# Optimization experiments

Measured on AMD Instinct MI355X. Metric: run time of the kernel, lower is better.

## Reference

```python
import jax, jax.numpy as jnp
import numpy as np

MARGIN = 2.0   # self.m
SCALE = 30.0   # cosine-head logit scale


def setup_inputs() -> dict:
    key = jax.random.key(0)
    k1, k2, k3 = jax.random.split(key, 3)
    B, D, C = 8192, 256, 5994
    emb = jax.random.normal(k1, (B, D), dtype=jnp.float32)
    W = jax.random.normal(k2, (C, D), dtype=jnp.float32) * 0.05
    y = jax.random.randint(k3, (B,), 0, C, dtype=jnp.int32)
    # first half domain 0 (main), second half domain 1 (target)
    y_d = jnp.concatenate([jnp.zeros(B // 2, jnp.int32), jnp.ones(B // 2, jnp.int32)])
    return {"emb": emb, "W": W, "y": y, "y_d": y_d}


def _clf_head(emb, W, y):
    # cosine-similarity classifier + cross-entropy (standard ASV clf head)
    e = emb / (jnp.linalg.norm(emb, axis=1, keepdims=True) + 1e-12)
    w = W / (jnp.linalg.norm(W, axis=1, keepdims=True) + 1e-12)
    logits = SCALE * (e @ w.T)                     # [B, C]
    logp = jax.nn.log_softmax(logits, axis=-1)
    loss = -jnp.mean(jnp.take_along_axis(logp, y[:, None], axis=1))
    acc = jnp.mean((jnp.argmax(logits, axis=-1) == y).astype(jnp.float32))
    return loss, acc


def reference(emb, W, y, y_d):
    B, D = emb.shape
    H = B // 2
    idx = jnp.arange(B)
    # faithful scatter: domain-0 rows -> main_emb[i]; domain-1 rows -> target_emb[i % H]
    # out-of-range sentinel H is dropped (rows with wrong domain stay zero)
    main_idx = jnp.where(y_d == 0, idx, H)
    tgt_idx = jnp.where(y_d != 0, idx % H, H)
    main_emb = jnp.zeros((H, D), emb.dtype).at[main_idx].set(emb, mode="drop")
    target_emb = jnp.zeros((H, D), emb.dtype).at[tgt_idx].set(emb, mode="drop")

    loss_c, acc = _clf_head(emb, W, y)

    # pairwise diffs: even rows main[i]-main[(i+1)%H] (label 1), odd rows main[i]-target[i] (label 0)
    pos_diff = main_emb - jnp.roll(main_emb, -1, axis=0)  # [H, D]
    neg_diff = main_emb - target_emb                      # [H, D]
    das_diff = jnp.stack([pos_diff, neg_diff], axis=1).reshape(B, D)
    das_label = jnp.tile(jnp.array([1.0, 0.0], emb.dtype), H)  # [B]

    das_dist = jnp.linalg.norm(das_diff, axis=1)
    das_loss = jnp.mean((1.0 - das_label) * das_dist ** 2
                        + das_label * jnp.maximum(MARGIN - das_dist, 0.0) ** 2)
    das_dist_mean = jnp.mean(jax.lax.stop_gradient(das_dist))
    return (loss_c, das_loss, acc, das_dist_mean)
```

## Files before the change

### kernel.cpp

```cpp
#include <hip/hip_runtime.h>
#include <hip/hip_bf16.h>

#define B_ROWS 8192
#define DIM 256
#define C_CLS 5994
#define N_CHUNK 188
#define NSPL 16
#define NPACK 444
#define NDAS 128
#define NMERGE 512
#define H_HALF 4096
#define SCALE_F 30.0f
#define MAXL 30.0f
#define EXPC 43.2808512266689f

#if defined(__has_builtin)
#if __has_builtin(__builtin_amdgcn_exp2f)
#define EXP2(x) __builtin_amdgcn_exp2f(x)
#endif
#endif
#ifndef EXP2
#define EXP2(x) exp2f(x)
#endif

typedef float f32x16 __attribute__((ext_vector_type(16)));
typedef long long ll;
typedef ll ll2 __attribute__((ext_vector_type(2)));

__global__ __launch_bounds__(256)
void k_pack(const float* __restrict__ emb, const float* __restrict__ W,
            char* __restrict__ en_blk, char* __restrict__ wn_blk,
            float* __restrict__ rne, float* __restrict__ rnw,
            unsigned* __restrict__ cnt) {
  __shared__ float ssm[256];
  __shared__ float rnl[32];
  const int b = blockIdx.x;
  const int t = threadIdx.x;
  if (b == 0 && t == 0) *cnt = 0u;
  const bool isW = b >= (B_ROWS/32);
  const int tile = isW ? b - (B_ROWS/32) : b;
  const int l31 = t & 31;
  const int row = tile*32 + l31;
  const float* __restrict__ src = isW ? W : emb;
  const bool rv = (!isW) || (row < C_CLS);

  float v[4][8];
  float ss = 0.f;
  #pragma unroll
  for (int i=0;i<4;i++) {
    const int d0 = ((t>>6) + i*4)*16 + ((t>>5)&1)*8;
    if (rv) {
      float4 x0 = *(const float4*)(src + (size_t)row*DIM + d0);
      float4 x1 = *(const float4*)(src + (size_t)row*DIM + d0 + 4);
      v[i][0]=x0.x; v[i][1]=x0.y; v[i][2]=x0.z; v[i][3]=x0.w;
      v[i][4]=x1.x; v[i][5]=x1.y; v[i][6]=x1.z; v[i][7]=x1.w;
      ss += x0.x*x0.x + x0.y*x0.y + x0.z*x0.z + x0.w*x0.w
          + x1.x*x1.x + x1.y*x1.y + x1.z*x1.z + x1.w*x1.w;
    } else {
      #pragma unroll
      for (int j=0;j<8;j++) v[i][j] = 0.f;
    }
  }
  ssm[t] = ss;
  __syncthreads();
  if (t < 32) {
    float s = 0.f;
    #pragma unroll
    for (int j=0;j<8;j++) s += ssm[t + j*32];
    float rn = 1.0f/(sqrtf(s) + 1e-12f);
    rnl[t] = rn;
    int rw = tile*32 + t;
    if (!isW) rne[rw] = rn;
    else if (rw < C_CLS) rnw[rw] = rn;
  }
  __syncthreads();
  const float rn = rnl[l31];
  char* __restrict__ dst = (isW ? wn_blk : en_blk) + (size_t)tile*8192;
  #pragma unroll
  for (int i=0;i<4;i++) {
    const int kk = (t>>6) + i*4;
    const int off = (kk>>1)*1024 + ((t>>5)&1)*512 + l31*16 + (kk&1)*8;
    int d0 = 0, d1 = 0;
    d0 = __builtin_amdgcn_cvt_pk_fp8_f32(v[i][0]*rn, v[i][1]*rn, d0, false);
    d0 = __builtin_amdgcn_cvt_pk_fp8_f32(v[i][2]*rn, v[i][3]*rn, d0, true);
    d1 = __builtin_amdgcn_cvt_pk_fp8_f32(v[i][4]*rn, v[i][5]*rn, d1, false);
    d1 = __builtin_amdgcn_cvt_pk_fp8_f32(v[i][6]*rn, v[i][7]*rn, d1, true);
    uint2 u; u.x = (unsigned)d0; u.y = (unsigned)d1;
    *(uint2*)(dst + off) = u;
  }
}

__global__ __launch_bounds__(256)
void k_das(const float* __restrict__ emb, const int* __restrict__ y_d,
           float* __restrict__ dasL, float* __restrict__ dasD) {
  __shared__ float s0[4], s1[4];
  const int wid = threadIdx.x >> 6, lane = threadIdx.x & 63;
  float a2 = 0.f, a3 = 0.f;
  for (int i = blockIdx.x*4 + wid; i < H_HALF; i += NDAS*4) {
    const int j = (i+1) & (H_HALF-1);
    const int di = y_d[i], dj = y_d[j], dih = y_d[i + H_HALF];
    float4 z = {0.f,0.f,0.f,0.f};
    float4 mi = (di==0)  ? *(const float4*)(emb + (size_t)i*DIM + lane*4) : z;
    float4 mj = (dj==0)  ? *(const float4*)(emb + (size_t)j*DIM + lane*4) : z;
    float4 ti = (dih!=0) ? *(const float4*)(emb + (size_t)(i+H_HALF)*DIM + lane*4)
                         : ((di!=0) ? *(const float4*)(emb + (size_t)i*DIM + lane*4) : z);
    float px = mi.x-mj.x, py = mi.y-mj.y, pz = mi.z-mj.z, pw = mi.w-mj.w;
    float nx = mi.x-ti.x, ny = mi.y-ti.y, nz = mi.z-ti.z, nw = mi.w-ti.w;
    float sp = px*px+py*py+pz*pz+pw*pw;
    float sn = nx*nx+ny*ny+nz*nz+nw*nw;
    #pragma unroll
    for (int off=1; off<64; off<<=1) { sp += __shfl_xor(sp, off); sn += __shfl_xor(sn, off); }
    if (lane == 0) {
      float dp = sqrtf(sp), dn = sqrtf(sn);
      float m = fmaxf(2.0f - dp, 0.f);
      a2 += m*m + dn*dn;
      a3 += dp + dn;
    }
  }
  if (lane == 0) { s0[wid] = a2; s1[wid] = a3; }
  __syncthreads();
  if (threadIdx.x == 0) {
    dasL[blockIdx.x] = s0[0]+s0[1]+s0[2]+s0[3];
    dasD[blockIdx.x] = s1[0]+s1[1]+s1[2]+s1[3];
  }
}

__global__ __launch_bounds__(256, 2)
void k_logits(const char* __restrict__ en_blk, const char* __restrict__ wn_blk,
              float* __restrict__ psum, unsigned* __restrict__ pkey) {
  const int split = blockIdx.x & (NSPL-1);
  const int panel = blockIdx.x / NSPL;
  const int wid  = threadIdx.x >> 6;
  const int lane = threadIdx.x & 63;
  const int l31  = lane & 31;
  const int tile = panel*4 + wid;

  ll2 a[8];
  const char* ab = en_blk + (size_t)tile*8192 + lane*16;
  #pragma unroll
  for (int j=0;j<8;j++) a[j] = *(const ll2*)(ab + j*1024);

  float ssum[16]; unsigned key[16];
  #pragma unroll
  for (int r=0;r<16;r++){ ssum[r]=0.f; key[r]=0u; }

  const int nit = (N_CHUNK - split + NSPL - 1) / NSPL;
  const char* p = wn_blk + (size_t)split*8192 + lane*16;
  const ptrdiff_t STEP = (ptrdiff_t)NSPL*8192;

  ll2 b0[4], b1[4];
  #pragma unroll
  for (int j=0;j<4;j++) b0[j] = *(const ll2*)(p + j*1024);
  #pragma unroll
  for (int j=0;j<4;j++) b1[j] = *(const ll2*)(p + (j+4)*1024);

  unsigned colu = (unsigned)(split*32 + l31);
  for (int it = 0; it < nit-1; ++it) {
    const char* pn = p + STEP;
    f32x16 acc = {};
    #pragma unroll
    for (int j=0;j<4;j++) {
      acc = __builtin_amdgcn_mfma_f32_32x32x16_fp8_fp8(a[j][0], b0[j][0], acc, 0,0,0);
      acc = __builtin_amdgcn_mfma_f32_32x32x16_fp8_fp8(a[j][1], b0[j][1], acc, 0,0,0);
    }
    #pragma unroll
    for (int j=0;j<4;j++) b0[j] = *(const ll2*)(pn + j*1024);
    #pragma unroll
    for (int j=0;j<4;j++) {
      acc = __builtin_amdgcn_mfma_f32_32x32x16_fp8_fp8(a[j+4][0], b1[j][0], acc, 0,0,0);
      acc = __builtin_amdgcn_mfma_f32_32x32x16_fp8_fp8(a[j+4][1], b1[j][1], acc, 0,0,0);
    }
    #pragma unroll
    for (int j=0;j<4;j++) b1[j] = *(const ll2*)(pn + (j+4)*1024);
    #pragma unroll
    for (int r=0;r<16;r++) {
      float x = acc[r];
      ssum[r] += EXP2(fmaf(x, EXPC, -EXPC));
      unsigned ky = (__float_as_uint(x + 2.0f) & 0xFFFFE000u) | colu;
      key[r] = ky > key[r] ? ky : key[r];
    }
    colu += NSPL*32;
    p = pn;
  }
  {
    f32x16 acc = {};
    #pragma unroll
    for (int j=0;j<4;j++) {
      acc = __builtin_amdgcn_mfma_f32_32x32x16_fp8_fp8(a[j][0], b0[j][0], acc, 0,0,0);
      acc = __builtin_amdgcn_mfma_f32_32x32x16_fp8_fp8(a[j][1], b0[j][1], acc, 0,0,0);
    }
    #pragma unroll
    for (int j=0;j<4;j++) {
      acc = __builtin_amdgcn_mfma_f32_32x32x16_fp8_fp8(a[j+4][0], b1[j][0], acc, 0,0,0);
      acc = __builtin_amdgcn_mfma_f32_32x32x16_fp8_fp8(a[j+4][1], b1[j][1], acc, 0,0,0);
    }
    #pragma unroll
    for (int r=0;r<16;r++) {
      float x = acc[r];
      ssum[r] += EXP2(fmaf(x, EXPC, -EXPC));
      unsigned ky = (__float_as_uint(x + 2.0f) & 0xFFFFE000u) | colu;
      key[r] = ky > key[r] ? ky : key[r];
    }
  }

  #pragma unroll
  for (int off=1; off<32; off<<=1) {
    #pragma unroll
    for (int r=0;r<16;r++) {
      ssum[r] += __shfl_xor(ssum[r], off);
      unsigned o = __shfl_xor(key[r], off);
      key[r] = o > key[r] ? o : key[r];
    }
  }
  if (l31 == 0) {
    const int rowbase = tile*32;
    #pragma unroll
    for (int r=0;r<16;r++) {
      int row = rowbase + (r&3) + 8*(r>>2) + 4*(lane>>5);
      psum[(size_t)row*NSPL + split] = ssum[r];
      pkey[(size_t)row*NSPL + split] = key[r];
    }
  }
}

__global__ __launch_bounds__(256)
void k_tail(const float* __restrict__ emb, const float* __restrict__ W,
            const int* __restrict__ y,
            const float* __restrict__ rne, const float* __restrict__ rnw,
            const float* __restrict__ psum, const unsigned* __restrict__ pkey,
            float* __restrict__ lossP, float* __restrict__ corrP,
            const float* __restrict__ dasL, const float* __restrict__ dasD,
            unsigned* __restrict__ cnt, float* __restrict__ out) {
  __shared__ float s0[4], s1[4];
  __shared__ int isLast;
  const int wid = threadIdx.x >> 6, lane = threadIdx.x & 63;
  float lacc = 0.f, cacc = 0.f;
  for (int row = blockIdx.x*4 + wid; row < B_ROWS; row += NMERGE*4) {
    const int yc = y[row];
    float4 e = *(const float4*)(emb + (size_t)row*DIM + lane*4);
    float4 w = *(const float4*)(W + (size_t)yc*DIM + lane*4);
    float d = e.x*w.x + e.y*w.y + e.z*w.z + e.w*w.w;
    #pragma unroll
    for (int off=1; off<64; off<<=1) d += __shfl_xor(d, off);
    float S = 0.f; unsigned km = 0u;
    if (lane < NSPL) {
      S = psum[(size_t)row*NSPL + lane];
      km = pkey[(size_t)row*NSPL + lane];
    }
    #pragma unroll
    for (int off=1; off<NSPL; off<<=1) {
      S += __shfl_xor(S, off);
      unsigned o = __shfl_xor(km, off);
      if (o > km) km = o;
    }
    if (lane == 0) {
      float ly = SCALE_F * d * rne[row] * rnw[yc];
      lacc += MAXL + logf(S) - ly;
      cacc += ((km & 0x1FFFu) == (unsigned)yc) ? 1.f : 0.f;
    }
  }
  if (lane == 0) { s0[wid] = lacc; s1[wid] = cacc; }
  __syncthreads();
  if (threadIdx.x == 0) {
    lossP[blockIdx.x] = s0[0]+s0[1]+s0[2]+s0[3];
    corrP[blockIdx.x] = s1[0]+s1[1]+s1[2]+s1[3];
    __threadfence();
    unsigned done = atomicAdd(cnt, 1u);
    isLast = (done == NMERGE-1u) ? 1 : 0;
  }
  __syncthreads();
  if (isLast) {
    const int t = threadIdx.x;
    float lv = atomicAdd(&lossP[t], 0.f) + atomicAdd(&lossP[t+256], 0.f);
    float cv = atomicAdd(&corrP[t], 0.f) + atomicAdd(&corrP[t+256], 0.f);
    float dl = (t < NDAS) ? atomicAdd((float*)&dasL[t], 0.f) : 0.f;
    float dd = (t < NDAS) ? atomicAdd((float*)&dasD[t], 0.f) : 0.f;
    #pragma unroll
    for (int off=1; off<64; off<<=1) {
      lv += __shfl_xor(lv, off); cv += __shfl_xor(cv, off);
      dl += __shfl_xor(dl, off); dd += __shfl_xor(dd, off);
    }
    __shared__ float r4[4][4];
    if (lane == 0) { r4[wid][0]=lv; r4[wid][1]=cv; r4[wid][2]=dl; r4[wid][3]=dd; }
    __syncthreads();
    if (t == 0) {
      out[0] = (r4[0][0]+r4[1][0]+r4[2][0]+r4[3][0]) * (1.0f/B_ROWS);
      out[1] = (r4[0][2]+r4[1][2]+r4[2][2]+r4[3][2]) * (1.0f/B_ROWS);
      out[2] = (r4[0][1]+r4[1][1]+r4[2][1]+r4[3][1]) * (1.0f/B_ROWS);
      out[3] = (r4[0][3]+r4[1][3]+r4[2][3]+r4[3][3]) * (1.0f/B_ROWS);
    }
  }
}

extern "C" void kernel_launch(void* const* d_in, const int* in_sizes, int n_in,
                              void* d_out, int out_size, void* d_ws, size_t ws_size,
                              hipStream_t stream) {
  const float* emb = (const float*)d_in[0];
  const float* W   = (const float*)d_in[1];
  const int*   y   = (const int*)d_in[2];
  const int*   y_d = (const int*)d_in[3];

  char* ws = (char*)d_ws;
  const size_t EN_OFF   = 0;
  const size_t WN_OFF   = EN_OFF  + (size_t)256*8192;
  const size_t RNE_OFF  = WN_OFF  + (size_t)N_CHUNK*8192;
  const size_t RNW_OFF  = RNE_OFF + (size_t)B_ROWS*4;
  const size_t PSUM_OFF = RNW_OFF + 24064;
  const size_t PKEY_OFF = PSUM_OFF + (size_t)NSPL*B_ROWS*4;
  const size_t LP_OFF   = PKEY_OFF + (size_t)NSPL*B_ROWS*4;
  const size_t CP_OFF   = LP_OFF   + NMERGE*4;
  const size_t DL_OFF   = CP_OFF   + NMERGE*4;
  const size_t DD_OFF   = DL_OFF   + NDAS*4;
  const size_t CNT_OFF  = DD_OFF   + NDAS*4;

  char*     en_blk = ws + EN_OFF;
  char*     wn_blk = ws + WN_OFF;
  float*    rne   = (float*)(ws + RNE_OFF);
  float*    rnw   = (float*)(ws + RNW_OFF);
  float*    psum  = (float*)(ws + PSUM_OFF);
  unsigned* pkey  = (unsigned*)(ws + PKEY_OFF);
  float*    lossP = (float*)(ws + LP_OFF);
  float*    corrP = (float*)(ws + CP_OFF);
  float*    dasL  = (float*)(ws + DL_OFF);
  float*    dasD  = (float*)(ws + DD_OFF);
  unsigned* cnt   = (unsigned*)(ws + CNT_OFF);

  k_pack<<<NPACK, 256, 0, stream>>>(emb, W, en_blk, wn_blk, rne, rnw, cnt);
  k_das<<<NDAS, 256, 0, stream>>>(emb, y_d, dasL, dasD);
  k_logits<<<64*NSPL, 256, 0, stream>>>(en_blk, wn_blk, psum, pkey);
  k_tail<<<NMERGE, 256, 0, stream>>>(emb, W, y, rne, rnw, psum, pkey,
                                     lossP, corrP, dasL, dasD, cnt, (float*)d_out);
}
```

Before: 71.14 us.

## Fuse DAS into pack kernel and capture target logit inside GEMM epilogue

The separate DAS kernel becomes extra blocks appended to the pack kernel, saving one launch and letting both run concurrently. The target-class logit is now taken from the fp8 MFMA accumulator during the logits pass and stored per split, instead of being recomputed in the tail from fp32 emb and W rows plus saved norms. This cuts the tail's global reads and the rne/rnw writes, but adds a compare/select per accumulator element in the hot loop and a third per-split output array. The target logit now carries fp8 precision rather than the previous fp32 dot product.

```diff
diff --git a/kernel.cpp b/kernel.cpp
--- a/kernel.cpp
+++ b/kernel.cpp
@@ -29,14 +29,51 @@
 
 __global__ __launch_bounds__(256)
 void k_pack(const float* __restrict__ emb, const float* __restrict__ W,
+            const int* __restrict__ y_d,
             char* __restrict__ en_blk, char* __restrict__ wn_blk,
-            float* __restrict__ rne, float* __restrict__ rnw,
+            float* __restrict__ dasL, float* __restrict__ dasD,
             unsigned* __restrict__ cnt) {
   __shared__ float ssm[256];
   __shared__ float rnl[32];
+  __shared__ float s0[4], s1[4];
   const int b = blockIdx.x;
   const int t = threadIdx.x;
   if (b == 0 && t == 0) *cnt = 0u;
+
+  if (b >= NPACK) {
+    const int bd = b - NPACK;
+    const int wid = t >> 6, lane = t & 63;
+    float a2 = 0.f, a3 = 0.f;
+    for (int i = bd*4 + wid; i < H_HALF; i += NDAS*4) {
+      const int j = (i+1) & (H_HALF-1);
+      const int di = y_d[i], dj = y_d[j], dih = y_d[i + H_HALF];
+      float4 z = {0.f,0.f,0.f,0.f};
+      float4 mi = (di==0)  ? *(const float4*)(emb + (size_t)i*DIM + lane*4) : z;
+      float4 mj = (dj==0)  ? *(const float4*)(emb + (size_t)j*DIM + lane*4) : z;
+      float4 ti = (dih!=0) ? *(const float4*)(emb + (size_t)(i+H_HALF)*DIM + lane*4)
+                           : ((di!=0) ? *(const float4*)(emb + (size_t)i*DIM + lane*4) : z);
+      float px = mi.x-mj.x, py = mi.y-mj.y, pz = mi.z-mj.z, pw = mi.w-mj.w;
+      float nx = mi.x-ti.x, ny = mi.y-ti.y, nz = mi.z-ti.z, nw = mi.w-ti.w;
+      float sp = px*px+py*py+pz*pz+pw*pw;
+      float sn = nx*nx+ny*ny+nz*nz+nw*nw;
+      #pragma unroll
+      for (int off=1; off<64; off<<=1) { sp += __shfl_xor(sp, off); sn += __shfl_xor(sn, off); }
+      if (lane == 0) {
+        float dp = sqrtf(sp), dn = sqrtf(sn);
+        float m = fmaxf(2.0f - dp, 0.f);
+        a2 += m*m + dn*dn;
+        a3 += dp + dn;
+      }
+    }
+    if (lane == 0) { s0[wid] = a2; s1[wid] = a3; }
+    __syncthreads();
+    if (t == 0) {
+      dasL[bd] = s0[0]+s0[1]+s0[2]+s0[3];
+      dasD[bd] = s1[0]+s1[1]+s1[2]+s1[3];
+    }
+    return;
+  }
+
   const bool isW = b >= (B_ROWS/32);
   const int tile = isW ? b - (B_ROWS/32) : b;
   const int l31 = t & 31;
@@ -67,11 +104,7 @@
     float s = 0.f;
     #pragma unroll
     for (int j=0;j<8;j++) s += ssm[t + j*32];
-    float rn = 1.0f/(sqrtf(s) + 1e-12f);
-    rnl[t] = rn;
-    int rw = tile*32 + t;
-    if (!isW) rne[rw] = rn;
-    else if (rw < C_CLS) rnw[rw] = rn;
+    rnl[t] = 1.0f/(sqrtf(s) + 1e-12f);
   }
   __syncthreads();
   const float rn = rnl[l31];
@@ -90,59 +123,33 @@
   }
 }
 
-__global__ __launch_bounds__(256)
-void k_das(const float* __restrict__ emb, const int* __restrict__ y_d,
-           float* __restrict__ dasL, float* __restrict__ dasD) {
-  __shared__ float s0[4], s1[4];
-  const int wid = threadIdx.x >> 6, lane = threadIdx.x & 63;
-  float a2 = 0.f, a3 = 0.f;
-  for (int i = blockIdx.x*4 + wid; i < H_HALF; i += NDAS*4) {
-    const int j = (i+1) & (H_HALF-1);
-    const int di = y_d[i], dj = y_d[j], dih = y_d[i + H_HALF];
-    float4 z = {0.f,0.f,0.f,0.f};
-    float4 mi = (di==0)  ? *(const float4*)(emb + (size_t)i*DIM + lane*4) : z;
-    float4 mj = (dj==0)  ? *(const float4*)(emb + (size_t)j*DIM + lane*4) : z;
-    float4 ti = (dih!=0) ? *(const float4*)(emb + (size_t)(i+H_HALF)*DIM + lane*4)
-                         : ((di!=0) ? *(const float4*)(emb + (size_t)i*DIM + lane*4) : z);
-    float px = mi.x-mj.x, py = mi.y-mj.y, pz = mi.z-mj.z, pw = mi.w-mj.w;
-    float nx = mi.x-ti.x, ny = mi.y-ti.y, nz = mi.z-ti.z, nw = mi.w-ti.w;
-    float sp = px*px+py*py+pz*pz+pw*pw;
-    float sn = nx*nx+ny*ny+nz*nz+nw*nw;
-    #pragma unroll
-    for (int off=1; off<64; off<<=1) { sp += __shfl_xor(sp, off); sn += __shfl_xor(sn, off); }
-    if (lane == 0) {
-      float dp = sqrtf(sp), dn = sqrtf(sn);
-      float m = fmaxf(2.0f - dp, 0.f);
-      a2 += m*m + dn*dn;
-      a3 += dp + dn;
-    }
-  }
-  if (lane == 0) { s0[wid] = a2; s1[wid] = a3; }
-  __syncthreads();
-  if (threadIdx.x == 0) {
-    dasL[blockIdx.x] = s0[0]+s0[1]+s0[2]+s0[3];
-    dasD[blockIdx.x] = s1[0]+s1[1]+s1[2]+s1[3];
-  }
-}
-
 __global__ __launch_bounds__(256, 2)
 void k_logits(const char* __restrict__ en_blk, const char* __restrict__ wn_blk,
-              float* __restrict__ psum, unsigned* __restrict__ pkey) {
+              const int* __restrict__ y,
+              float* __restrict__ psum, unsigned* __restrict__ pkey,
+              float* __restrict__ lyP) {
   const int split = blockIdx.x & (NSPL-1);
   const int panel = blockIdx.x / NSPL;
   const int wid  = threadIdx.x >> 6;
   const int lane = threadIdx.x & 63;
   const int l31  = lane & 31;
+  const int lh   = lane >> 5;
   const int tile = panel*4 + wid;
+  const int rowbase = tile*32;
 
   ll2 a[8];
   const char* ab = en_blk + (size_t)tile*8192 + lane*16;
   #pragma unroll
   for (int j=0;j<8;j++) a[j] = *(const ll2*)(ab + j*1024);
 
-  float ssum[16]; unsigned key[16];
-  #pragma unroll
-  for (int r=0;r<16;r++){ ssum[r]=0.f; key[r]=0u; }
+  unsigned tcol[16];
+  #pragma unroll
+  for (int r=0;r<16;r++)
+    tcol[r] = (unsigned)y[rowbase + (r&3) + 8*(r>>2) + 4*lh];
+
+  float ssum[16], lyv[16]; unsigned key[16];
+  #pragma unroll
+  for (int r=0;r<16;r++){ ssum[r]=0.f; key[r]=0u; lyv[r]=-3.0e38f; }
 
   const int nit = (N_CHUNK - split + NSPL - 1) / NSPL;
   const char* p = wn_blk + (size_t)split*8192 + lane*16;
@@ -178,6 +185,7 @@
       ssum[r] += EXP2(fmaf(x, EXPC, -EXPC));
       unsigned ky = (__float_as_uint(x + 2.0f) & 0xFFFFE000u) | colu;
       key[r] = ky > key[r] ? ky : key[r];
+      lyv[r] = (colu == tcol[r]) ? x : lyv[r];
     }
     colu += NSPL*32;
     p = pn;
@@ -200,6 +208,7 @@
       ssum[r] += EXP2(fmaf(x, EXPC, -EXPC));
       unsigned ky = (__float_as_uint(x + 2.0f) & 0xFFFFE000u) | colu;
       key[r] = ky > key[r] ? ky : key[r];
+      lyv[r] = (colu == tcol[r]) ? x : lyv[r];
     }
   }
 
@@ -210,24 +219,24 @@
       ssum[r] += __shfl_xor(ssum[r], off);
       unsigned o = __shfl_xor(key[r], off);
       key[r] = o > key[r] ? o : key[r];
+      lyv[r] = fmaxf(lyv[r], __shfl_xor(lyv[r], off));
     }
   }
   if (l31 == 0) {
-    const int rowbase = tile*32;
     #pragma unroll
     for (int r=0;r<16;r++) {
-      int row = rowbase + (r&3) + 8*(r>>2) + 4*(lane>>5);
+      int row = rowbase + (r&3) + 8*(r>>2) + 4*lh;
       psum[(size_t)row*NSPL + split] = ssum[r];
       pkey[(size_t)row*NSPL + split] = key[r];
+      lyP [(size_t)row*NSPL + split] = lyv[r];
     }
   }
 }
 
 __global__ __launch_bounds__(256)
-void k_tail(const float* __restrict__ emb, const float* __restrict__ W,
-            const int* __restrict__ y,
-            const float* __restrict__ rne, const float* __restrict__ rnw,
+void k_tail(const int* __restrict__ y,
             const float* __restrict__ psum, const unsigned* __restrict__ pkey,
+            const float* __restrict__ lyP,
             float* __restrict__ lossP, float* __restrict__ corrP,
             const float* __restrict__ dasL, const float* __restrict__ dasD,
             unsigned* __restrict__ cnt, float* __restrict__ out) {
@@ -236,27 +245,22 @@
   const int wid = threadIdx.x >> 6, lane = threadIdx.x & 63;
   float lacc = 0.f, cacc = 0.f;
   for (int row = blockIdx.x*4 + wid; row < B_ROWS; row += NMERGE*4) {
-    const int yc = y[row];
-    float4 e = *(const float4*)(emb + (size_t)row*DIM + lane*4);
-    float4 w = *(const float4*)(W + (size_t)yc*DIM + lane*4);
-    float d = e.x*w.x + e.y*w.y + e.z*w.z + e.w*w.w;
-    #pragma unroll
-    for (int off=1; off<64; off<<=1) d += __shfl_xor(d, off);
-    float S = 0.f; unsigned km = 0u;
+    float S = 0.f, lym = -3.0e38f; unsigned km = 0u;
     if (lane < NSPL) {
-      S = psum[(size_t)row*NSPL + lane];
-      km = pkey[(size_t)row*NSPL + lane];
+      S   = psum[(size_t)row*NSPL + lane];
+      km  = pkey[(size_t)row*NSPL + lane];
+      lym = lyP [(size_t)row*NSPL + lane];
     }
     #pragma unroll
     for (int off=1; off<NSPL; off<<=1) {
       S += __shfl_xor(S, off);
       unsigned o = __shfl_xor(km, off);
       if (o > km) km = o;
+      lym = fmaxf(lym, __shfl_xor(lym, off));
     }
     if (lane == 0) {
-      float ly = SCALE_F * d * rne[row] * rnw[yc];
-      lacc += MAXL + logf(S) - ly;
-      cacc += ((km & 0x1FFFu) == (unsigned)yc) ? 1.f : 0.f;
+      lacc += MAXL + logf(S) - SCALE_F * lym;
+      cacc += ((km & 0x1FFFu) == (unsigned)y[row]) ? 1.f : 0.f;
     }
   }
   if (lane == 0) { s0[wid] = lacc; s1[wid] = cacc; }
@@ -271,8 +275,8 @@
   __syncthreads();
   if (isLast) {
     const int t = threadIdx.x;
-    float lv = atomicAdd(&lossP[t], 0.f) + atomicAdd(&lossP[t+256], 0.f);
-    float cv = atomicAdd(&corrP[t], 0.f) + atomicAdd(&corrP[t+256], 0.f);
+    float lv = atomicAdd((float*)&lossP[t], 0.f) + atomicAdd((float*)&lossP[t+256], 0.f);
+    float cv = atomicAdd((float*)&corrP[t], 0.f) + atomicAdd((float*)&corrP[t+256], 0.f);
     float dl = (t < NDAS) ? atomicAdd((float*)&dasL[t], 0.f) : 0.f;
     float dd = (t < NDAS) ? atomicAdd((float*)&dasD[t], 0.f) : 0.f;
     #pragma unroll
@@ -303,11 +307,10 @@
   char* ws = (char*)d_ws;
   const size_t EN_OFF   = 0;
   const size_t WN_OFF   = EN_OFF  + (size_t)256*8192;
-  const size_t RNE_OFF  = WN_OFF  + (size_t)N_CHUNK*8192;
-  const size_t RNW_OFF  = RNE_OFF + (size_t)B_ROWS*4;
-  const size_t PSUM_OFF = RNW_OFF + 24064;
+  const size_t PSUM_OFF = WN_OFF  + (size_t)N_CHUNK*8192;
   const size_t PKEY_OFF = PSUM_OFF + (size_t)NSPL*B_ROWS*4;
-  const size_t LP_OFF   = PKEY_OFF + (size_t)NSPL*B_ROWS*4;
+  const size_t LY_OFF   = PKEY_OFF + (size_t)NSPL*B_ROWS*4;
+  const size_t LP_OFF   = LY_OFF   + (size_t)NSPL*B_ROWS*4;
   const size_t CP_OFF   = LP_OFF   + NMERGE*4;
   const size_t DL_OFF   = CP_OFF   + NMERGE*4;
   const size_t DD_OFF   = DL_OFF   + NDAS*4;
@@ -315,19 +318,17 @@
 
   char*     en_blk = ws + EN_OFF;
   char*     wn_blk = ws + WN_OFF;
-  float*    rne   = (float*)(ws + RNE_OFF);
-  float*    rnw   = (float*)(ws + RNW_OFF);
   float*    psum  = (float*)(ws + PSUM_OFF);
   unsigned* pkey  = (unsigned*)(ws + PKEY_OFF);
+  float*    lyP   = (float*)(ws + LY_OFF);
   float*    lossP = (float*)(ws + LP_OFF);
   float*    corrP = (float*)(ws + CP_OFF);
   float*    dasL  = (float*)(ws + DL_OFF);
   float*    dasD  = (float*)(ws + DD_OFF);
   unsigned* cnt   = (unsigned*)(ws + CNT_OFF);
 
-  k_pack<<<NPACK, 256, 0, stream>>>(emb, W, en_blk, wn_blk, rne, rnw, cnt);
-  k_das<<<NDAS, 256, 0, stream>>>(emb, y_d, dasL, dasD);
-  k_logits<<<64*NSPL, 256, 0, stream>>>(en_blk, wn_blk, psum, pkey);
-  k_tail<<<NMERGE, 256, 0, stream>>>(emb, W, y, rne, rnw, psum, pkey,
-                                     lossP, corrP, dasL, dasD, cnt, (float*)d_out);
+  k_pack<<<NPACK + NDAS, 256, 0, stream>>>(emb, W, y_d, en_blk, wn_blk, dasL, dasD, cnt);
+  k_logits<<<64*NSPL, 256, 0, stream>>>(en_blk, wn_blk, y, psum, pkey, lyP);
+  k_tail<<<NMERGE, 256, 0, stream>>>(y, psum, pkey, lyP, lossP, corrP,
+                                     dasL, dasD, cnt, (float*)d_out);
 }
```

Result: no change. 72.18 us (+1.5%).
